# Optimization experiments

Hardware: AMD Instinct MI355X
Metric: run time of the kernel (lower is better)

The kernel has to match this reference:

```python
import jax, jax.numpy as jnp
import numpy as np

N_NODES = 100000
N_EDGES = 1600000
EPS = 1e-5  # nn.BatchNorm1d default eps


def setup_inputs() -> dict:
    key = jax.random.key(0)
    ks = jax.random.split(key, 6)
    x = jax.random.normal(ks[0], (N_NODES, 11), dtype=jnp.float32)
    edge_index = jax.random.randint(ks[1], (2, N_EDGES), 0, N_NODES, dtype=jnp.int64)
    edge_weight = jax.random.uniform(ks[2], (N_EDGES,), dtype=jnp.float32)
    W1 = jax.random.normal(ks[3], (11, 64), dtype=jnp.float32) * 0.3
    b1 = jnp.zeros((64,), dtype=jnp.float32)
    gamma = jnp.ones((64,), dtype=jnp.float32)
    beta = jnp.zeros((64,), dtype=jnp.float32)
    W2 = jax.random.normal(ks[4], (64, 128), dtype=jnp.float32) * 0.125
    b2 = jnp.zeros((128,), dtype=jnp.float32)
    return {"x": x, "edge_index": edge_index, "edge_weight": edge_weight,
            "W1": W1, "b1": b1, "gamma": gamma, "beta": beta, "W2": W2, "b2": b2}


def _gcn_conv(x, row, col, w, W, b, n_nodes):
    """PyG GCNConv: h = x @ W; symmetric-norm aggregate at col; + bias.
    row/col/w already include self loops (weight 1.0)."""
    h = x @ W  # [N, F_out]
    deg = jax.ops.segment_sum(w, col, num_segments=n_nodes)  # [N]
    dinv = jnp.where(deg > 0, jax.lax.rsqrt(jnp.maximum(deg, 1e-12)), 0.0)
    norm = dinv[row] * w * dinv[col]  # [E+N]
    msg = h[row] * norm[:, None]  # gather + scale, [E+N, F_out]
    out = jax.ops.segment_sum(msg, col, num_segments=n_nodes)  # scatter-add
    return out + b


def _batch_norm(x, gamma, beta):
    # training-mode BatchNorm1d over node dimension, biased variance
    mean = jnp.mean(x, axis=0)
    var = jnp.mean(jnp.square(x - mean), axis=0)
    return (x - mean) * jax.lax.rsqrt(var + EPS) * gamma + beta


def reference(x, edge_index, edge_weight, W1, b1, gamma, beta, W2, b2):
    n = x.shape[0]
    loops = jnp.arange(n, dtype=edge_index.dtype)
    row = jnp.concatenate([edge_index[0], loops])
    col = jnp.concatenate([edge_index[1], loops])
    w = jnp.concatenate([edge_weight, jnp.ones((n,), dtype=edge_weight.dtype)])

    h = _gcn_conv(x, row, col, w, W1, b1, n)
    h = _batch_norm(h, gamma, beta)
    h = jax.nn.relu(h)
    # dropout is identity at inference (deterministic baseline)
    out = _gcn_conv(h, row, col, w, W2, b2, n)
    return out
```

## Files before the change

### kernel.cpp

```cpp
#include <hip/hip_runtime.h>

#define F0 11
#define F1 64
#define F2 128
#define TN2 128

#define CHUNKS 64
#define BPR 12544
#define WPR (BPR / 2)
#define NBS 1024

__device__ __forceinline__ unsigned short f2bf(float v) {
  unsigned u = __float_as_uint(v);
  unsigned r = u + 0x7FFFu + ((u >> 16) & 1u);
  return (unsigned short)(r >> 16);
}
__device__ __forceinline__ float bf2f(unsigned short s) {
  return __uint_as_float(((unsigned)s) << 16);
}
__device__ __forceinline__ float bf2f_lo(unsigned v) {
  return __uint_as_float(v << 16);
}
__device__ __forceinline__ float bf2f_hi(unsigned v) {
  return __uint_as_float(v & 0xFFFF0000u);
}

__global__ void k_pad(const float* __restrict__ x, unsigned short* __restrict__ x16b, int n) {
  int i = blockIdx.x * blockDim.x + threadIdx.x;
  if (i >= n * 16) return;
  int r = i >> 4, f = i & 15;
  x16b[i] = (f < F0) ? f2bf(x[(size_t)r * F0 + f]) : (unsigned short)0;
}

__global__ __launch_bounds__(1024) void k_hist(const int* __restrict__ col,
                                               unsigned* __restrict__ partial,
                                               int E, int CE, int N, int ranges) {
  __shared__ unsigned lds[WPR];
  int r = blockIdx.x % ranges;
  int c = blockIdx.x / ranges;
  int lo = r * BPR;
  int hi = min(N, lo + BPR);
  int t = threadIdx.x;
  for (int i = t; i < WPR; i += 1024) lds[i] = 0;
  __syncthreads();
  int e0 = c * CE, e1 = min(E, e0 + CE);
  for (int e = e0 + t; e < e1; e += 1024) {
    int b = col[e];
    if (b >= lo && b < hi) {
      int local = b - lo;
      atomicAdd(&lds[local >> 1], 1u << (16 * (local & 1)));
    }
  }
  __syncthreads();
  unsigned* dst = partial + ((size_t)r * CHUNKS + c) * WPR;
  for (int i = t; i < WPR; i += 1024) dst[i] = lds[i];
}

__global__ void k_colprefix(const unsigned* __restrict__ partial,
                            unsigned short* __restrict__ rel,
                            int* __restrict__ cnt, int N, int npad) {
  int bin = blockIdx.x * blockDim.x + threadIdx.x;
  if (bin >= N) return;
  int r = bin / BPR, local = bin % BPR;
  int word = local >> 1, sh = 16 * (local & 1);
  const unsigned* p = partial + (size_t)r * CHUNKS * WPR + word;
  unsigned acc = 0;
  for (int c = 0; c < CHUNKS; c++) {
    unsigned v = (p[(size_t)c * WPR] >> sh) & 0xFFFFu;
    rel[(size_t)c * npad + bin] = (unsigned short)acc;
    acc += v;
  }
  cnt[bin] = (int)acc;
}

__global__ void k_scan1(const int* __restrict__ cnt, int* __restrict__ offs,
                        int* __restrict__ bsum, int n) {
  __shared__ int s[1024];
  int tid = threadIdx.x;
  int i = blockIdx.x * 1024 + tid;
  int v = (i < n) ? cnt[i] : 0;
  s[tid] = v;
  __syncthreads();
  for (int d = 1; d < 1024; d <<= 1) {
    int t = (tid >= d) ? s[tid - d] : 0;
    __syncthreads();
    s[tid] += t;
    __syncthreads();
  }
  if (i < n) offs[i] = s[tid] - v;
  if (tid == 1023) bsum[blockIdx.x] = s[1023];
}

__global__ void k_scan2(int* __restrict__ bsum, int nb) {
  __shared__ int s[256];
  __shared__ int carry;
  int t = threadIdx.x;
  if (t == 0) carry = 0;
  __syncthreads();
  for (int base = 0; base < nb; base += 256) {
    int v = (base + t < nb) ? bsum[base + t] : 0;
    s[t] = v;
    __syncthreads();
    for (int d = 1; d < 256; d <<= 1) {
      int x = (t >= d) ? s[t - d] : 0;
      __syncthreads();
      s[t] += x;
      __syncthreads();
    }
    int total = s[255];
    if (base + t < nb) bsum[base + t] = carry + s[t] - v;
    __syncthreads();
    if (t == 0) carry += total;
    __syncthreads();
  }
}

__global__ void k_scan3(int* __restrict__ offs, const int* __restrict__ bsum,
                        int n, int total) {
  int i = blockIdx.x * 1024 + threadIdx.x;
  if (i < n) offs[i] += bsum[blockIdx.x];
  if (i == 0) offs[n] = total;
}

__global__ __launch_bounds__(1024) void k_fill(const int* __restrict__ row,
                                               const int* __restrict__ col,
                                               const float* __restrict__ w,
                                               const int* __restrict__ offs,
                                               const unsigned short* __restrict__ rel,
                                               uint2* __restrict__ csr8,
                                               int E, int CE, int N, int npad, int ranges) {
  __shared__ unsigned cur[WPR];
  int r = blockIdx.x % ranges;
  int c = blockIdx.x / ranges;
  int lo = r * BPR;
  int hi = min(N, lo + BPR);
  int t = threadIdx.x;
  const unsigned* rsrc = (const unsigned*)(rel + (size_t)c * npad + lo);
  int nw = (hi - lo + 1) >> 1;
  for (int i = t; i < nw; i += 1024) cur[i] = rsrc[i];
  __syncthreads();
  int e0 = c * CE, e1 = min(E, e0 + CE);
  for (int e = e0 + t; e < e1; e += 1024) {
    int b = col[e];
    if (b >= lo && b < hi) {
      int local = b - lo;
      int sh = 16 * (local & 1);
      unsigned old = atomicAdd(&cur[local >> 1], 1u << sh);
      unsigned myrel = (old >> sh) & 0xFFFFu;
      int pos = offs[b] + (int)myrel;
      csr8[pos] = make_uint2((unsigned)row[e], __float_as_uint(w[e]));
    }
  }
}

__global__ void k_deg2(const uint2* __restrict__ csr8, const int* __restrict__ offs,
                       float* __restrict__ dinv, int n) {
  int wid = (blockIdx.x * blockDim.x + threadIdx.x) >> 6;
  int lane = threadIdx.x & 63;
  if (wid >= n) return;
  int s = offs[wid], e = offs[wid + 1];
  float acc = 0.f;
  for (int k = s + lane; k < e; k += 64) acc += __uint_as_float(csr8[k].y);
#pragma unroll
  for (int d = 32; d > 0; d >>= 1) acc += __shfl_down(acc, d);
  if (lane == 0) dinv[wid] = rsqrtf(1.0f + acc);
}

__global__ void k_norm(uint2* __restrict__ csr8, const float* __restrict__ dinv, int E) {
  int i = blockIdx.x * blockDim.x + threadIdx.x;
  if (i >= E) return;
  uint2 v = csr8[i];
  csr8[i].y = __float_as_uint(dinv[v.x] * __uint_as_float(v.y));
}

__global__ void k_agg1g(const unsigned short* __restrict__ x16b, const int* __restrict__ offs,
                        const uint2* __restrict__ csr8, const float* __restrict__ dinv,
                        const float* __restrict__ W1, const float* __restrict__ b1,
                        unsigned short* __restrict__ h, int n) {
  __shared__ float Ws[F0 * F1];
  __shared__ float bs[F1];
  __shared__ unsigned s_soff[4][64];
  __shared__ float    s_nrm[4][64];
  int t = threadIdx.x;
  for (int i = t; i < F0 * F1; i += 256) Ws[i] = W1[i];
  if (t < F1) bs[t] = b1[t];
  __syncthreads();
  int wv = t >> 6;
  int lane = t & 63;
  int wid = (blockIdx.x * blockDim.x + t) >> 6;
  if (wid >= n) return;
  int g = lane >> 4, f = lane & 15;
  float di = dinv[wid];
  float a0 = (g == 0) ? di * bf2f(x16b[(size_t)wid * 16 + f]) : 0.f;
  float a1 = 0.f, a2 = 0.f, a3 = 0.f;
  int s = offs[wid], e = offs[wid + 1];
  for (int base = s; base < e; base += 64) {
    int m = e - base; if (m > 64) m = 64;
    if (lane < m) {
      uint2 v = csr8[base + lane];
      s_soff[wv][lane] = v.x * 16u;
      s_nrm[wv][lane] = __uint_as_float(v.y);
    } else {
      s_soff[wv][lane] = 0u;
      s_nrm[wv][lane] = 0.f;
    }
    int mp = (m + 15) & ~15;
    for (int jb = 0; jb < mp; jb += 16) {
      unsigned o0 = s_soff[wv][jb + g],      o1 = s_soff[wv][jb + 4 + g];
      unsigned o2 = s_soff[wv][jb + 8 + g],  o3 = s_soff[wv][jb + 12 + g];
      float    m0 = s_nrm[wv][jb + g],       m1 = s_nrm[wv][jb + 4 + g];
      float    m2 = s_nrm[wv][jb + 8 + g],   m3 = s_nrm[wv][jb + 12 + g];
      a0 += m0 * bf2f(x16b[(size_t)o0 + f]);
      a1 += m1 * bf2f(x16b[(size_t)o1 + f]);
      a2 += m2 * bf2f(x16b[(size_t)o2 + f]);
      a3 += m3 * bf2f(x16b[(size_t)o3 + f]);
    }
  }
  float acc = (a0 + a1) + (a2 + a3);
  acc += __shfl_xor(acc, 16);
  acc += __shfl_xor(acc, 32);
  float av = di * acc;
  float o = bs[lane];
#pragma unroll
  for (int k = 0; k < F0; k++) o += __shfl(av, k) * Ws[k * F1 + lane];
  h[(size_t)wid * F1 + lane] = f2bf(o);
}

__global__ void k_bn_stats(const unsigned short* __restrict__ h, float2* __restrict__ pbn,
                           int total4) {
  int t = threadIdx.x;
  int idx = blockIdx.x * blockDim.x + t;
  int stride = gridDim.x * blockDim.x;
  const uint2* hp = (const uint2*)h;
  float s0 = 0, s1 = 0, s2 = 0, s3 = 0, q0 = 0, q1 = 0, q2 = 0, q3 = 0;
  for (int i = idx; i < total4; i += stride) {
    uint2 v = hp[i];
    float a = bf2f_lo(v.x), b = bf2f_hi(v.x);
    float c = bf2f_lo(v.y), d = bf2f_hi(v.y);
    s0 += a; q0 += a * a;
    s1 += b; q1 += b * b;
    s2 += c; q2 += c * c;
    s3 += d; q3 += d * d;
  }
  __shared__ float ss[256][4], qq[256][4];
  ss[t][0] = s0; ss[t][1] = s1; ss[t][2] = s2; ss[t][3] = s3;
  qq[t][0] = q0; qq[t][1] = q1; qq[t][2] = q2; qq[t][3] = q3;
  __syncthreads();
  if (t < 64) {
    int o = t >> 2, sub = t & 3;
    float S = 0.f, Q = 0.f;
#pragma unroll
    for (int i = 0; i < 16; i++) {
      S += ss[o + 16 * i][sub];
      Q += qq[o + 16 * i][sub];
    }
    pbn[(size_t)blockIdx.x * 64 + t] = make_float2(S, Q);
  }
}

__global__ void k_bn_mid(const float2* __restrict__ pbn, float2* __restrict__ pbn2) {
  __shared__ float sS[4][64], sQ[4][64];
  int t = threadIdx.x;
  int f = t & 63, g = t >> 6;
  int b0 = blockIdx.x * 16;
  float S = 0.f, Q = 0.f;
  for (int b = b0 + g; b < b0 + 16; b += 4) {
    float2 v = pbn[(size_t)b * 64 + f];
    S += v.x; Q += v.y;
  }
  sS[g][f] = S; sQ[g][f] = Q;
  __syncthreads();
  if (t < 64)
    pbn2[(size_t)blockIdx.x * 64 + t] =
        make_float2(sS[0][t] + sS[1][t] + sS[2][t] + sS[3][t],
                    sQ[0][t] + sQ[1][t] + sQ[2][t] + sQ[3][t]);
}

__global__ void k_bn_final(const float2* __restrict__ pbn2, const float* __restrict__ gamma,
                           const float* __restrict__ beta, float* __restrict__ scalef,
                           float* __restrict__ shiftf, int n) {
  __shared__ double sS[4][64], sQ[4][64];
  int t = threadIdx.x;
  int f = t & 63, g = t >> 6;
  double S = 0.0, Q = 0.0;
  for (int b = g; b < 64; b += 4) {
    float2 v = pbn2[(size_t)b * 64 + f];
    S += v.x; Q += v.y;
  }
  sS[g][f] = S; sQ[g][f] = Q;
  __syncthreads();
  if (t < 64) {
    double SS = sS[0][t] + sS[1][t] + sS[2][t] + sS[3][t];
    double QQ = sQ[0][t] + sQ[1][t] + sQ[2][t] + sQ[3][t];
    double mean = SS / (double)n;
    double var = QQ / (double)n - mean * mean;
    if (var < 0.0) var = 0.0;
    float scale = gamma[t] * (float)(1.0 / sqrt(var + 1e-5));
    scalef[t] = scale;
    shiftf[t] = beta[t] - (float)mean * scale;
  }
}

__global__ void k_agg2(const unsigned short* __restrict__ h, const int* __restrict__ offs,
                       const uint2* __restrict__ csr8, const float* __restrict__ dinv,
                       const float* __restrict__ scalef, const float* __restrict__ shiftf,
                       float* __restrict__ agg2, int n) {
  __shared__ unsigned s_soff[4][64];
  __shared__ float    s_nrm[4][64];
  int t = threadIdx.x;
  int wv = t >> 6;
  int lane = t & 63;
  int wid = (blockIdx.x * blockDim.x + t) >> 6;
  if (wid >= n) return;
  float sc = scalef[lane], sf = shiftf[lane];
  float di = dinv[wid];
  float a0 = di * fmaxf(fmaf(bf2f(h[(size_t)wid * F1 + lane]), sc, sf), 0.f);
  float a1 = 0.f, a2 = 0.f, a3 = 0.f;
  int s = offs[wid], e = offs[wid + 1];
  for (int base = s; base < e; base += 64) {
    int m = e - base; if (m > 64) m = 64;
    if (lane < m) {
      uint2 v = csr8[base + lane];
      s_soff[wv][lane] = v.x * 64u;
      s_nrm[wv][lane] = __uint_as_float(v.y);
    } else {
      s_soff[wv][lane] = 0u;
      s_nrm[wv][lane] = 0.f;
    }
    int mp = (m + 3) & ~3;
    for (int j = 0; j < mp; j += 4) {
      unsigned o0 = s_soff[wv][j + 0], o1 = s_soff[wv][j + 1];
      unsigned o2 = s_soff[wv][j + 2], o3 = s_soff[wv][j + 3];
      float m0 = s_nrm[wv][j + 0], m1 = s_nrm[wv][j + 1];
      float m2 = s_nrm[wv][j + 2], m3 = s_nrm[wv][j + 3];
      a0 += m0 * fmaxf(fmaf(bf2f(h[(size_t)o0 + lane]), sc, sf), 0.f);
      a1 += m1 * fmaxf(fmaf(bf2f(h[(size_t)o1 + lane]), sc, sf), 0.f);
      a2 += m2 * fmaxf(fmaf(bf2f(h[(size_t)o2 + lane]), sc, sf), 0.f);
      a3 += m3 * fmaxf(fmaf(bf2f(h[(size_t)o3 + lane]), sc, sf), 0.f);
    }
  }
  agg2[(size_t)wid * F1 + lane] = di * ((a0 + a1) + (a2 + a3));
}

__global__ __launch_bounds__(256) void k_gemm2(const float* __restrict__ agg2,
                                               const float* __restrict__ W2,
                                               const float* __restrict__ b2,
                                               float* __restrict__ out, int n) {
  __shared__ float Ws[F1 * F2];
  __shared__ float As[F1][TN2];
  int t = threadIdx.x;
  for (int i = t; i < F1 * F2 / 4; i += 256) ((float4*)Ws)[i] = ((const float4*)W2)[i];
  int nb = blockIdx.x * TN2;
  int node = t & 127;
  int kh = (t >> 7) * 32;
  int gnode = nb + node;
  if (gnode < n) {
    const float4* src = (const float4*)(agg2 + (size_t)gnode * F1 + kh);
#pragma unroll
    for (int j = 0; j < 8; j++) {
      float4 v = src[j];
      As[kh + j * 4 + 0][node] = v.x;
      As[kh + j * 4 + 1][node] = v.y;
      As[kh + j * 4 + 2][node] = v.z;
      As[kh + j * 4 + 3][node] = v.w;
    }
  } else {
#pragma unroll
    for (int j = 0; j < 8; j++) {
      As[kh + j * 4 + 0][node] = 0.f;
      As[kh + j * 4 + 1][node] = 0.f;
      As[kh + j * 4 + 2][node] = 0.f;
      As[kh + j * 4 + 3][node] = 0.f;
    }
  }
  __syncthreads();

  int f0 = (t & 15) * 8;
  int n0 = (t >> 4) * 8;
  float acc[8][8];
  float bv[8];
#pragma unroll
  for (int j = 0; j < 8; j++) bv[j] = b2[f0 + j];
#pragma unroll
  for (int i = 0; i < 8; i++)
#pragma unroll
    for (int j = 0; j < 8; j++) acc[i][j] = bv[j];

#pragma unroll 4
  for (int k = 0; k < F1; k++) {
    float4 a0 = *(const float4*)&As[k][n0];
    float4 a1 = *(const float4*)&As[k][n0 + 4];
    float4 w0 = *(const float4*)&Ws[k * F2 + f0];
    float4 w1 = *(const float4*)&Ws[k * F2 + f0 + 4];
    float a[8] = {a0.x, a0.y, a0.z, a0.w, a1.x, a1.y, a1.z, a1.w};
    float w[8] = {w0.x, w0.y, w0.z, w0.w, w1.x, w1.y, w1.z, w1.w};
#pragma unroll
    for (int i = 0; i < 8; i++)
#pragma unroll
      for (int j = 0; j < 8; j++) acc[i][j] += a[i] * w[j];
  }

#pragma unroll
  for (int i = 0; i < 8; i++) {
    int gi = nb + n0 + i;
    if (gi < n) {
      float4 o0 = {acc[i][0], acc[i][1], acc[i][2], acc[i][3]};
      float4 o1 = {acc[i][4], acc[i][5], acc[i][6], acc[i][7]};
      *(float4*)&out[(size_t)gi * F2 + f0] = o0;
      *(float4*)&out[(size_t)gi * F2 + f0 + 4] = o1;
    }
  }
}

extern "C" void kernel_launch(void* const* d_in, const int* in_sizes, int n_in,
                              void* d_out, int out_size, void* d_ws, size_t ws_size,
                              hipStream_t stream) {
  const float* x     = (const float*)d_in[0];
  const int*   ei    = (const int*)d_in[1];
  const float* ew    = (const float*)d_in[2];
  const float* W1    = (const float*)d_in[3];
  const float* b1    = (const float*)d_in[4];
  const float* gamma = (const float*)d_in[5];
  const float* beta  = (const float*)d_in[6];
  const float* W2    = (const float*)d_in[7];
  const float* b2    = (const float*)d_in[8];
  float* out = (float*)d_out;

  int N = in_sizes[0] / F0;
  int E = in_sizes[1] / 2;
  const int* row = ei;
  const int* col = ei + E;
  if (N <= 0) return;

  int CE = (E + CHUNKS - 1) / CHUNKS;
  int RANGES = (N + BPR - 1) / BPR;
  int npad = RANGES * BPR;

  char* p = (char*)d_ws;
  auto alloc = [&](size_t bytes) -> void* {
    void* r = (void*)p;
    p += (bytes + 255) & ~(size_t)255;
    return r;
  };
  size_t partial_bytes = ((size_t)RANGES * CHUNKS * WPR * 4 + 255) & ~(size_t)255;
  size_t rel_bytes     = (size_t)CHUNKS * npad * 2;
  size_t h_bytes       = (size_t)N * F1 * 2;
  size_t region_bytes  = partial_bytes + rel_bytes;
  if (h_bytes > region_bytes) region_bytes = h_bytes;

  float*          dinv    = (float*)alloc((size_t)N * 4);
  int*            cnt     = (int*)alloc((size_t)N * 4);
  int*            offs    = (int*)alloc((size_t)(N + 1) * 4);
  int             NB      = (N + 1023) / 1024;
  int*            bsum    = (int*)alloc((size_t)NB * 4);
  uint2*          csr8    = (uint2*)alloc((size_t)E * 8);
  char*           region  = (char*)alloc(region_bytes);
  unsigned*       partial = (unsigned*)region;
  unsigned short* rel     = (unsigned short*)(region + partial_bytes);
  unsigned short* h       = (unsigned short*)region;
  unsigned short* x16b    = (unsigned short*)alloc((size_t)N * 16 * 2);
  float*          agg2    = (float*)alloc((size_t)N * F1 * 4);
  float2*         pbn     = (float2*)alloc((size_t)NBS * 64 * 8);
  float2*         pbn2    = (float2*)alloc((size_t)64 * 64 * 8);
  float*          scalef  = (float*)alloc(64 * 4);
  float*          shiftf  = (float*)alloc(64 * 4);
  (void)ws_size; (void)n_in; (void)out_size;

  int bW = (N + 3) / 4;
  int bG2 = (N + TN2 - 1) / TN2;
  int gRC = CHUNKS * RANGES;

  k_pad<<<(N * 16 + 255) / 256, 256, 0, stream>>>(x, x16b, N);
  k_hist<<<gRC, 1024, 0, stream>>>(col, partial, E, CE, N, RANGES);
  k_colprefix<<<(N + 255) / 256, 256, 0, stream>>>(partial, rel, cnt, N, npad);
  k_scan1<<<NB, 1024, 0, stream>>>(cnt, offs, bsum, N);
  k_scan2<<<1, 256, 0, stream>>>(bsum, NB);
  k_scan3<<<NB, 1024, 0, stream>>>(offs, bsum, N, E);
  k_fill<<<gRC, 1024, 0, stream>>>(row, col, ew, offs, rel, csr8, E, CE, N, npad, RANGES);
  k_deg2<<<bW, 256, 0, stream>>>(csr8, offs, dinv, N);
  k_norm<<<(E + 255) / 256, 256, 0, stream>>>(csr8, dinv, E);
  k_agg1g<<<bW, 256, 0, stream>>>(x16b, offs, csr8, dinv, W1, b1, h, N);
  k_bn_stats<<<NBS, 256, 0, stream>>>(h, pbn, N * F1 / 4);
  k_bn_mid<<<64, 256, 0, stream>>>(pbn, pbn2);
  k_bn_final<<<1, 256, 0, stream>>>(pbn2, gamma, beta, scalef, shiftf, N);
  k_agg2<<<bW, 256, 0, stream>>>(h, offs, csr8, dinv, scalef, shiftf, agg2, N);
  k_gemm2<<<bG2, 256, 0, stream>>>(agg2, W2, b2, out, N);
}
```

Before: 247.3 us.

## Add nontemporal loads, two nodes per wave in agg1, deeper unroll in agg2

Streaming reads of col/row/w, the partial histograms and the CSR entries now use nontemporal load/store builtins so they do not pollute cache. The first aggregation kernel maps two nodes per 64-lane wave (32 lanes each), halving its grid and reducing idle lanes for low-degree nodes. The second aggregation kernel unrolls the neighbor loop to 8 independent accumulators for more memory-level parallelism. The bn_stats load is reworked as a 64-bit scalar load. The changes are mixed micro-optimizations whose effects may offset each other, for example nontemporal hints may hurt if the data would otherwise be reused from L2.

```diff
diff --git a/kernel.cpp b/kernel.cpp
--- a/kernel.cpp
+++ b/kernel.cpp
@@ -9,6 +9,13 @@
 #define BPR 12544
 #define WPR (BPR / 2)
 #define NBS 1024
+
+#define NTL(p) __builtin_nontemporal_load(p)
+
+__device__ __forceinline__ uint2 ntl_u2(const uint2* p) {
+  unsigned long long v = __builtin_nontemporal_load((const unsigned long long*)p);
+  return make_uint2((unsigned)v, (unsigned)(v >> 32));
+}
 
 __device__ __forceinline__ unsigned short f2bf(float v) {
   unsigned u = __float_as_uint(v);
@@ -45,7 +52,7 @@
   __syncthreads();
   int e0 = c * CE, e1 = min(E, e0 + CE);
   for (int e = e0 + t; e < e1; e += 1024) {
-    int b = col[e];
+    int b = NTL(&col[e]);
     if (b >= lo && b < hi) {
       int local = b - lo;
       atomicAdd(&lds[local >> 1], 1u << (16 * (local & 1)));
@@ -53,7 +60,7 @@
   }
   __syncthreads();
   unsigned* dst = partial + ((size_t)r * CHUNKS + c) * WPR;
-  for (int i = t; i < WPR; i += 1024) dst[i] = lds[i];
+  for (int i = t; i < WPR; i += 1024) __builtin_nontemporal_store(lds[i], &dst[i]);
 }
 
 __global__ void k_colprefix(const unsigned* __restrict__ partial,
@@ -66,7 +73,7 @@
   const unsigned* p = partial + (size_t)r * CHUNKS * WPR + word;
   unsigned acc = 0;
   for (int c = 0; c < CHUNKS; c++) {
-    unsigned v = (p[(size_t)c * WPR] >> sh) & 0xFFFFu;
+    unsigned v = (NTL(&p[(size_t)c * WPR]) >> sh) & 0xFFFFu;
     rel[(size_t)c * npad + bin] = (unsigned short)acc;
     acc += v;
   }
@@ -137,18 +144,20 @@
   int t = threadIdx.x;
   const unsigned* rsrc = (const unsigned*)(rel + (size_t)c * npad + lo);
   int nw = (hi - lo + 1) >> 1;
-  for (int i = t; i < nw; i += 1024) cur[i] = rsrc[i];
+  for (int i = t; i < nw; i += 1024) cur[i] = NTL(&rsrc[i]);
   __syncthreads();
   int e0 = c * CE, e1 = min(E, e0 + CE);
   for (int e = e0 + t; e < e1; e += 1024) {
-    int b = col[e];
+    int b = NTL(&col[e]);
     if (b >= lo && b < hi) {
       int local = b - lo;
       int sh = 16 * (local & 1);
       unsigned old = atomicAdd(&cur[local >> 1], 1u << sh);
       unsigned myrel = (old >> sh) & 0xFFFFu;
       int pos = offs[b] + (int)myrel;
-      csr8[pos] = make_uint2((unsigned)row[e], __float_as_uint(w[e]));
+      int rv = NTL(&row[e]);
+      float wv = NTL(&w[e]);
+      csr8[pos] = make_uint2((unsigned)rv, __float_as_uint(wv));
     }
   }
 }
@@ -187,29 +196,37 @@
   __syncthreads();
   int wv = t >> 6;
   int lane = t & 63;
-  int wid = (blockIdx.x * blockDim.x + t) >> 6;
-  if (wid >= n) return;
-  int g = lane >> 4, f = lane & 15;
-  float di = dinv[wid];
-  float a0 = (g == 0) ? di * bf2f(x16b[(size_t)wid * 16 + f]) : 0.f;
+  int wid2 = (blockIdx.x * blockDim.x + t) >> 6;
+  int half = lane >> 5;
+  int hl = lane & 31;
+  int node = wid2 * 2 + half;
+  bool valid = node < n;
+  int nd = valid ? node : 0;
+  int g2 = hl >> 4, f = lane & 15;
+  float di = valid ? dinv[nd] : 0.f;
+  int s = valid ? offs[nd] : 0;
+  int e = valid ? offs[nd + 1] : 0;
+  float a0 = (g2 == 0) ? di * bf2f(x16b[(size_t)nd * 16 + f]) : 0.f;
   float a1 = 0.f, a2 = 0.f, a3 = 0.f;
-  int s = offs[wid], e = offs[wid + 1];
-  for (int base = s; base < e; base += 64) {
-    int m = e - base; if (m > 64) m = 64;
-    if (lane < m) {
-      uint2 v = csr8[base + lane];
+  int len = e - s;
+  int b0 = half * 32;
+  for (int base = 0; base < len; base += 32) {
+    int m = len - base; if (m > 32) m = 32;
+    if (hl < m) {
+      uint2 v = ntl_u2(&csr8[s + base + hl]);
       s_soff[wv][lane] = v.x * 16u;
       s_nrm[wv][lane] = __uint_as_float(v.y);
     } else {
       s_soff[wv][lane] = 0u;
       s_nrm[wv][lane] = 0.f;
     }
-    int mp = (m + 15) & ~15;
-    for (int jb = 0; jb < mp; jb += 16) {
-      unsigned o0 = s_soff[wv][jb + g],      o1 = s_soff[wv][jb + 4 + g];
-      unsigned o2 = s_soff[wv][jb + 8 + g],  o3 = s_soff[wv][jb + 12 + g];
-      float    m0 = s_nrm[wv][jb + g],       m1 = s_nrm[wv][jb + 4 + g];
-      float    m2 = s_nrm[wv][jb + 8 + g],   m3 = s_nrm[wv][jb + 12 + g];
+    int mp = (m + 7) & ~7;
+    for (int jb = 0; jb < mp; jb += 8) {
+      int j0 = b0 + jb + g2;
+      unsigned o0 = s_soff[wv][j0 + 0], o1 = s_soff[wv][j0 + 2];
+      unsigned o2 = s_soff[wv][j0 + 4], o3 = s_soff[wv][j0 + 6];
+      float    m0 = s_nrm[wv][j0 + 0],  m1 = s_nrm[wv][j0 + 2];
+      float    m2 = s_nrm[wv][j0 + 4],  m3 = s_nrm[wv][j0 + 6];
       a0 += m0 * bf2f(x16b[(size_t)o0 + f]);
       a1 += m1 * bf2f(x16b[(size_t)o1 + f]);
       a2 += m2 * bf2f(x16b[(size_t)o2 + f]);
@@ -218,12 +235,18 @@
   }
   float acc = (a0 + a1) + (a2 + a3);
   acc += __shfl_xor(acc, 16);
-  acc += __shfl_xor(acc, 32);
   float av = di * acc;
-  float o = bs[lane];
-#pragma unroll
-  for (int k = 0; k < F0; k++) o += __shfl(av, k) * Ws[k * F1 + lane];
-  h[(size_t)wid * F1 + lane] = f2bf(o);
+  float oA = bs[hl], oB = bs[hl + 32];
+#pragma unroll
+  for (int k = 0; k < F0; k++) {
+    float a = __shfl(av, (lane & 32) + k);
+    oA += a * Ws[k * F1 + hl];
+    oB += a * Ws[k * F1 + 32 + hl];
+  }
+  if (valid) {
+    h[(size_t)nd * F1 + hl] = f2bf(oA);
+    h[(size_t)nd * F1 + 32 + hl] = f2bf(oB);
+  }
 }
 
 __global__ void k_bn_stats(const unsigned short* __restrict__ h, float2* __restrict__ pbn,
@@ -231,12 +254,13 @@
   int t = threadIdx.x;
   int idx = blockIdx.x * blockDim.x + t;
   int stride = gridDim.x * blockDim.x;
-  const uint2* hp = (const uint2*)h;
+  const unsigned long long* hp = (const unsigned long long*)h;
   float s0 = 0, s1 = 0, s2 = 0, s3 = 0, q0 = 0, q1 = 0, q2 = 0, q3 = 0;
   for (int i = idx; i < total4; i += stride) {
-    uint2 v = hp[i];
-    float a = bf2f_lo(v.x), b = bf2f_hi(v.x);
-    float c = bf2f_lo(v.y), d = bf2f_hi(v.y);
+    unsigned long long vv = hp[i];
+    unsigned vx = (unsigned)vv, vy = (unsigned)(vv >> 32);
+    float a = bf2f_lo(vx), b = bf2f_hi(vx);
+    float c = bf2f_lo(vy), d = bf2f_hi(vy);
     s0 += a; q0 += a * a;
     s1 += b; q1 += b * b;
     s2 += c; q2 += c * c;
@@ -315,31 +339,40 @@
   float sc = scalef[lane], sf = shiftf[lane];
   float di = dinv[wid];
   float a0 = di * fmaxf(fmaf(bf2f(h[(size_t)wid * F1 + lane]), sc, sf), 0.f);
-  float a1 = 0.f, a2 = 0.f, a3 = 0.f;
+  float a1 = 0.f, a2 = 0.f, a3 = 0.f, a4 = 0.f, a5 = 0.f, a6 = 0.f, a7 = 0.f;
   int s = offs[wid], e = offs[wid + 1];
   for (int base = s; base < e; base += 64) {
     int m = e - base; if (m > 64) m = 64;
     if (lane < m) {
-      uint2 v = csr8[base + lane];
+      uint2 v = ntl_u2(&csr8[base + lane]);
       s_soff[wv][lane] = v.x * 64u;
       s_nrm[wv][lane] = __uint_as_float(v.y);
     } else {
       s_soff[wv][lane] = 0u;
       s_nrm[wv][lane] = 0.f;
     }
-    int mp = (m + 3) & ~3;
-    for (int j = 0; j < mp; j += 4) {
+    int mp = (m + 7) & ~7;
+    for (int j = 0; j < mp; j += 8) {
       unsigned o0 = s_soff[wv][j + 0], o1 = s_soff[wv][j + 1];
       unsigned o2 = s_soff[wv][j + 2], o3 = s_soff[wv][j + 3];
+      unsigned o4 = s_soff[wv][j + 4], o5 = s_soff[wv][j + 5];
+      unsigned o6 = s_soff[wv][j + 6], o7 = s_soff[wv][j + 7];
       float m0 = s_nrm[wv][j + 0], m1 = s_nrm[wv][j + 1];
       float m2 = s_nrm[wv][j + 2], m3 = s_nrm[wv][j + 3];
+      float m4 = s_nrm[wv][j + 4], m5 = s_nrm[wv][j + 5];
+      float m6 = s_nrm[wv][j + 6], m7 = s_nrm[wv][j + 7];
       a0 += m0 * fmaxf(fmaf(bf2f(h[(size_t)o0 + lane]), sc, sf), 0.f);
       a1 += m1 * fmaxf(fmaf(bf2f(h[(size_t)o1 + lane]), sc, sf), 0.f);
       a2 += m2 * fmaxf(fmaf(bf2f(h[(size_t)o2 + lane]), sc, sf), 0.f);
       a3 += m3 * fmaxf(fmaf(bf2f(h[(size_t)o3 + lane]), sc, sf), 0.f);
-    }
-  }
-  agg2[(size_t)wid * F1 + lane] = di * ((a0 + a1) + (a2 + a3));
+      a4 += m4 * fmaxf(fmaf(bf2f(h[(size_t)o4 + lane]), sc, sf), 0.f);
+      a5 += m5 * fmaxf(fmaf(bf2f(h[(size_t)o5 + lane]), sc, sf), 0.f);
+      a6 += m6 * fmaxf(fmaf(bf2f(h[(size_t)o6 + lane]), sc, sf), 0.f);
+      a7 += m7 * fmaxf(fmaf(bf2f(h[(size_t)o7 + lane]), sc, sf), 0.f);
+    }
+  }
+  agg2[(size_t)wid * F1 + lane] =
+      di * (((a0 + a1) + (a2 + a3)) + ((a4 + a5) + (a6 + a7)));
 }
 
 __global__ __launch_bounds__(256) void k_gemm2(const float* __restrict__ agg2,
@@ -466,7 +499,8 @@
   float*          shiftf  = (float*)alloc(64 * 4);
   (void)ws_size; (void)n_in; (void)out_size;
 
-  int bW = (N + 3) / 4;
+  int bW  = (N + 3) / 4;
+  int bW1 = ((N + 1) / 2 + 3) / 4;
   int bG2 = (N + TN2 - 1) / TN2;
   int gRC = CHUNKS * RANGES;
 
@@ -479,7 +513,7 @@
   k_fill<<<gRC, 1024, 0, stream>>>(row, col, ew, offs, rel, csr8, E, CE, N, npad, RANGES);
   k_deg2<<<bW, 256, 0, stream>>>(csr8, offs, dinv, N);
   k_norm<<<(E + 255) / 256, 256, 0, stream>>>(csr8, dinv, E);
-  k_agg1g<<<bW, 256, 0, stream>>>(x16b, offs, csr8, dinv, W1, b1, h, N);
+  k_agg1g<<<bW1, 256, 0, stream>>>(x16b, offs, csr8, dinv, W1, b1, h, N);
   k_bn_stats<<<NBS, 256, 0, stream>>>(h, pbn, N * F1 / 4);
   k_bn_mid<<<64, 256, 0, stream>>>(pbn, pbn2);
   k_bn_final<<<1, 256, 0, stream>>>(pbn2, gamma, beta, scalef, shiftf, N);
```

Result: slower. 273.6 us (+10.6%).
